# Kernel tuning notes

Hardware: AMD Instinct MI355X
Metric: run time of the kernel (lower is better)

The kernel has to match this reference:

```python
import jax, jax.numpy as jnp
import numpy as np

B, T, N = 4, 6, 1024          # patients, visits, diagnosis codes
CS, GS, H, AT, DA = 48, 32, 270, 32, 64  # code_size, graph_size, hidden, t_attention, dot-attn size
E, L, EV, ED = 32, 32, 20000, 400        # events/visit, event seq len, event vocab, event emb dim
OUT = 4000
INV_SQRT_AT = 1.0 / float(np.sqrt(AT))


def _w(k, shape, s=0.1):
    return jax.random.normal(k, shape, jnp.float32) * s


def setup_inputs():
    key = jax.random.key(0)
    ks = jax.random.split(key, 40)
    cat = jax.random.randint(ks[0], (B, T, N), 0, 4)  # disjoint m1/m2/m3 masks
    return {
        'code_x': jax.random.randint(ks[1], (B, T, N), 0, 2).astype(jnp.int32),
        'divided': jnp.stack([cat == 1, cat == 2, cat == 3], axis=-1).astype(jnp.int32),
        'neighbors': jax.random.randint(ks[2], (B, T, N), 0, 2).astype(jnp.int32),
        'lens': jnp.full((B,), T, dtype=jnp.int32),
        'events': jax.random.randint(ks[3], (B, T, E, L), 0, EV).astype(jnp.int32),
        'c_emb': _w(ks[4], (N, CS)),
        'n_emb': _w(ks[5], (N, CS)),
        'u_emb': _w(ks[6], (N, GS)),
        'adj': (jax.random.uniform(ks[7], (N, N)) < 0.02).astype(jnp.float32),
        'Wg': _w(ks[8], (CS, GS), 0.05), 'bg': jnp.zeros((GS,), jnp.float32),
        'gru_Wih': _w(ks[9], (GS, 3 * H), 0.05),
        'gru_Whh': _w(ks[10], (H, 3 * H), 0.05),
        'gru_bih': jnp.zeros((3 * H,), jnp.float32),
        'gru_bhh': jnp.zeros((3 * H,), jnp.float32),
        'Wq': _w(ks[11], (GS, AT), 0.05), 'bq': jnp.zeros((AT,), jnp.float32),
        'Wk': _w(ks[12], (GS, AT), 0.05), 'bk': jnp.zeros((AT,), jnp.float32),
        'Wv': _w(ks[13], (GS, H), 0.05), 'bv': jnp.zeros((H,), jnp.float32),
        'Wd': _w(ks[14], (H, DA), 0.05), 'bd': jnp.zeros((DA,), jnp.float32),
        'ctx': _w(ks[15], (DA,), 0.1),
        'Eemb': _w(ks[16], (EV, ED), 0.1),
        'lstm_Wih': _w(ks[17], (ED, 4 * H), 0.05),
        'lstm_Whh': _w(ks[18], (H, 4 * H), 0.05),
        'lstm_b': jnp.zeros((4 * H,), jnp.float32),
        'Wc': _w(ks[19], (H, OUT), 0.05),
        'bc': jnp.zeros((OUT,), jnp.float32),
    }


def _forward(code_x, divided, neighbors, events,
             c_emb, n_emb, u_emb, adj, Wg, bg,
             gru_Wih, gru_Whh, gru_bih, gru_bhh,
             Wq, bq, Wk, bk, Wv, bv,
             Wd, bd, ctx,
             Eemb, lstm_Wih, lstm_Whh, lstm_b,
             Wc, bc):
    Bsz, Tn, Nn = code_x.shape
    Hh = gru_Whh.shape[0]
    cx = code_x.astype(jnp.float32)
    nb = neighbors.astype(jnp.float32)
    dv = divided.astype(jnp.float32)

    def gru_cell(x, h):  # torch GRUCell: gates in (r, z, n) order
        gi = x @ gru_Wih + gru_bih
        gh = h @ gru_Whh + gru_bhh
        ir, iz, i_n = jnp.split(gi, 3, axis=-1)
        hr, hz, h_n = jnp.split(gh, 3, axis=-1)
        r = jax.nn.sigmoid(ir + hr)
        z = jax.nn.sigmoid(iz + hz)
        n = jnp.tanh(i_n + r * h_n)
        return (1.0 - z) * n + z * h

    def visit_step(carry, xs):
        h_prev, no_prev = carry
        t, c_t, n_t, d_t = xs  # c_t/n_t: [B,N], d_t: [B,N,3]
        cm = c_t[..., None]
        nm = n_t[..., None]
        # GraphLayer
        ce = cm * c_emb  # [B,N,CS]
        ne = nm * n_emb
        Ace = jnp.einsum('mn,bnc->bmc', adj, ce)
        Ane = jnp.einsum('mn,bnc->bmc', adj, ne)
        co = jax.nn.leaky_relu((ce + cm * Ace + cm * Ane) @ Wg + bg)  # [B,N,GS]
        no = jax.nn.leaky_relu((ne + nm * Ane + nm * Ace) @ Wg + bg)
        m1 = d_t[..., 0] > 0
        m2 = d_t[..., 1] > 0
        m3 = d_t[..., 2] > 0
        # TransitionLayer: persistent codes (m1) -> GRU, masked max-pool
        h_m1 = gru_cell(co, h_prev)  # [B,N,H]
        has1 = jnp.any(m1, axis=1, keepdims=True)
        mx1 = jnp.max(jnp.where(m1[..., None], h_m1, -jnp.inf), axis=1)
        out_m1 = jnp.where(has1, mx1, 0.0)
        # emerging (m2) / unrelated (m3) codes -> single-head attention over the m23 set
        m23 = m2 | m3
        q_in = jnp.where(m3[..., None], u_emb, no_prev)  # [B,N,GS]
        q = q_in @ Wq + bq
        k = co @ Wk + bk
        v = co @ Wv + bv
        g = jnp.einsum('bia,bja->bij', q, k) * INV_SQRT_AT  # [B,N,N]
        has23 = jnp.any(m23, axis=1)  # [B]
        g = jnp.where(m23[:, None, :], g, -jnp.inf)
        g = jnp.where(has23[:, None, None], g, 0.0)  # keep softmax finite when m23 empty
        score = jax.nn.softmax(g, axis=-1)
        h_m23 = jnp.tanh(jnp.einsum('bij,bjh->bih', score, v))  # [B,N,H]
        valid23 = (t > 0) & has23
        mx23 = jnp.max(jnp.where(m23[..., None], h_m23, -jnp.inf), axis=1)
        out_m23 = jnp.where(valid23[:, None], mx23, 0.0)
        h_new = jnp.where(m1[..., None], h_m1, 0.0)
        h_new = jnp.where(((t > 0) & m23)[..., None], h_m23, h_new)
        return (h_new, no), out_m1 + out_m23

    h0 = jnp.zeros((Bsz, Nn, Hh), jnp.float32)
    no0 = jnp.zeros((Bsz, Nn, GS), jnp.float32)
    xs = (jnp.arange(Tn), jnp.swapaxes(cx, 0, 1), jnp.swapaxes(nb, 0, 1), jnp.swapaxes(dv, 0, 1))
    _, outs = jax.lax.scan(visit_step, (h0, no0), xs)
    out_last = outs[-1]  # only the last visit's output survives the original loop

    # SentimentModel: embedding + LSTM over last visit's events (seqs == padded length L)
    x_emb = Eemb[events[:, -1]]  # [B,E,L,ED]

    def lstm_step(carry, x_t):  # torch LSTM gate order (i, f, g, o)
        h, c = carry
        gates = x_t @ lstm_Wih + h @ lstm_Whh + lstm_b
        i, f, gg, o = jnp.split(gates, 4, axis=-1)
        c = jax.nn.sigmoid(f) * c + jax.nn.sigmoid(i) * jnp.tanh(gg)
        h = jax.nn.sigmoid(o) * jnp.tanh(c)
        return (h, c), None

    hc0 = (jnp.zeros((Bsz, E, Hh), jnp.float32), jnp.zeros((Bsz, E, Hh), jnp.float32))
    (h_ev, _), _ = jax.lax.scan(lstm_step, hc0, jnp.moveaxis(x_emb, 2, 0))  # [B,E,H]

    def dp_attention(x):  # x: [B,M,H] -> [B,H]
        vu = (x @ Wd + bd) @ ctx  # [B,M]
        s = jax.nn.softmax(vu, axis=-1)
        return jnp.sum(x * s[..., None], axis=-2)

    stacked = jnp.concatenate([out_last[:, None, :], h_ev], axis=1)  # [B,1+E,H]
    o1 = dp_attention(stacked)
    o2 = dp_attention(o1[:, None, :])  # softmax over a singleton -> identity (as in source)
    return jax.nn.sigmoid(o2 @ Wc + bc)  # [B,OUT]


def reference(code_x, divided, neighbors, lens, events,
              c_emb, n_emb, u_emb, adj, Wg, bg,
              gru_Wih, gru_Whh, gru_bih, gru_bhh,
              Wq, bq, Wk, bk, Wv, bv,
              Wd, bd, ctx,
              Eemb, lstm_Wih, lstm_Whh, lstm_b,
              Wc, bc):
    # lens is all-T (fixed number of visits per patient in this reference)
    return _forward(code_x, divided, neighbors, events,
                    c_emb, n_emb, u_emb, adj, Wg, bg,
                    gru_Wih, gru_Whh, gru_bih, gru_bhh,
                    Wq, bq, Wk, bk, Wv, bv,
                    Wd, bd, ctx,
                    Eemb, lstm_Wih, lstm_Whh, lstm_b,
                    Wc, bc)
```

## Files before the change

kernel.cpp:

```cpp
#include <hip/hip_runtime.h>
#include <hip/hip_bf16.h>
#include <math.h>

#define Bc   4
#define Tc   6
#define Nc   1024
#define CSc  48
#define GSc  32
#define Hc   270
#define ATc  32
#define DAc  64
#define Ec   32
#define Lc   32
#define EDc  400
#define OUTc 4000
#define H3c  810
#define H4c  1080
#define BEc  128
#define KPE  416
#define KPG  64
#define KAB  320
#define NCMB 1382
#define NZCAP 96
#define INV_SQRT_AT_F 0.17677669529663687f

typedef unsigned short ushort_t;
using s8v  = __attribute__((ext_vector_type(8))) short;
using f4v  = __attribute__((ext_vector_type(4))) float;
using u16x8= __attribute__((ext_vector_type(8))) unsigned short;

__device__ __forceinline__ float sigmoid_f(float x){ return 1.0f/(1.0f+expf(-x)); }
__device__ __forceinline__ ushort_t f2bf(float x){
    __hip_bfloat16 b = __float2bfloat16(x);
    return *reinterpret_cast<ushort_t*>(&b);
}
__device__ __forceinline__ float b2f(ushort_t u){
    return __uint_as_float(((unsigned int)u)<<16);
}

template<int EPIL, int SPLITK, int ASEL>
__global__ __launch_bounds__(256)
void mfma_k(const ushort_t* __restrict__ A, const ushort_t* __restrict__ BT,
            const float* __restrict__ bias,
            void* __restrict__ P0, void* __restrict__ P1, void* __restrict__ P2,
            const float* __restrict__ PF, const int* __restrict__ DV,
            const int* __restrict__ DV2,
            int M, int N, int Kp, int lda, int ldb, int ldc,
            long long sA, long long sB, long long sC, int tpar)
{
    __shared__ ushort_t As[128*40];
    __shared__ ushort_t Bs[128*40];
    const int z = blockIdx.z;
    int kbeg = 0, kend = Kp;
    if (SPLITK > 0){
        int ks = Kp / SPLITK;
        kbeg = z*ks; kend = kbeg + ks;
    } else {
        if (ASEL == 0) A += (size_t)z * (size_t)sA;
        BT += (size_t)z * (size_t)sB;
    }
    const int m0 = blockIdx.y*128, n0 = blockIdx.x*128;
    const int tid = threadIdx.x;
    const int w = tid>>6, l = tid&63;
    const int wm = (w>>1)*64, wn = (w&1)*64;
    const int lr = l&15, lk = (l>>4)*8, lq = l>>4;
    const int srow = tid>>2, kseg = tid&3;

    f4v acc[4][4];
    #pragma unroll
    for (int mi=0;mi<4;mi++)
      #pragma unroll
      for (int ni=0;ni<4;ni++)
        acc[mi][ni] = (f4v){0.0f,0.0f,0.0f,0.0f};

    for (int k0=kbeg;k0<kend;k0+=32){
        #pragma unroll
        for (int i=0;i<2;i++){
            int row = srow + i*64;
            int ga = m0+row;
            uint4 va = make_uint4(0u,0u,0u,0u);
            if (ga < M){
                if (ASEL == 2){
                    int isno = ga >> 12;
                    int r = ga & 4095; int b = r >> 10, n = r & 1023;
                    int kk = k0 + kseg*8;
                    if (kk < CSc){
                        const float* emb = isno ? (const float*)P2 : (const float*)A;
                        const int*   msk = isno ? DV2 : DV;
                        float m = (float)msk[((size_t)b*Tc + tpar)*Nc + n];
                        f4v e0 = *(const f4v*)(emb + (size_t)n*CSc + kk);
                        f4v e1 = *(const f4v*)(emb + (size_t)n*CSc + kk + 4);
                        f4v s0 = *(const f4v*)(PF + (size_t)n*(Bc*CSc) + b*CSc + kk);
                        f4v s1 = *(const f4v*)(PF + (size_t)n*(Bc*CSc) + b*CSc + kk + 4);
                        u16x8 tmp;
                        #pragma unroll
                        for (int j=0;j<4;j++) tmp[j]   = f2bf(m*(e0[j]+s0[j]));
                        #pragma unroll
                        for (int j=0;j<4;j++) tmp[4+j] = f2bf(m*(e1[j]+s1[j]));
                        va = *(uint4*)&tmp;
                    }
                } else if (ASEL == 3){
                    int ll = ga >> 7, be = ga & 127; int b = be >> 5, e = be & 31;
                    int kk = k0 + kseg*8;
                    if (kk < EDc){
                        int ev = DV[(((size_t)b*Tc + (Tc-1))*Ec + e)*Lc + ll];
                        const float* src = PF + (size_t)ev*EDc + kk;
                        f4v e0 = *(const f4v*)src;
                        f4v e1 = *(const f4v*)(src + 4);
                        u16x8 tmp;
                        #pragma unroll
                        for (int j=0;j<4;j++) tmp[j]   = f2bf(e0[j]);
                        #pragma unroll
                        for (int j=0;j<4;j++) tmp[4+j] = f2bf(e1[j]);
                        va = *(uint4*)&tmp;
                    }
                } else {
                    va = *(const uint4*)(A + (size_t)ga*lda + k0 + kseg*8);
                }
            }
            *(uint4*)&As[row*40 + kseg*8] = va;
            int gb = n0+row;
            uint4 vb = make_uint4(0u,0u,0u,0u);
            if (gb < N) vb = *(const uint4*)(BT + (size_t)gb*ldb + k0 + kseg*8);
            *(uint4*)&Bs[row*40 + kseg*8] = vb;
        }
        __syncthreads();
        s8v af[4], bfr[4];
        #pragma unroll
        for (int mi=0;mi<4;mi++) af[mi]  = *(const s8v*)&As[(wm+mi*16+lr)*40 + lk];
        #pragma unroll
        for (int ni=0;ni<4;ni++) bfr[ni] = *(const s8v*)&Bs[(wn+ni*16+lr)*40 + lk];
        #pragma unroll
        for (int mi=0;mi<4;mi++)
          #pragma unroll
          for (int ni=0;ni<4;ni++)
            acc[mi][ni] = __builtin_amdgcn_mfma_f32_16x16x32_bf16(af[mi], bfr[ni], acc[mi][ni], 0,0,0);
        __syncthreads();
    }

    #pragma unroll
    for (int mi=0;mi<4;mi++){
      #pragma unroll
      for (int ni=0;ni<4;ni++){
        int col = n0+wn+ni*16+lr;
        if (col >= N) continue;
        float bv_ = bias ? bias[col] : 0.0f;
        #pragma unroll
        for (int r=0;r<4;r++){
          int row = m0+wm+mi*16+lq*4+r;
          if (row >= M) continue;
          float x = acc[mi][ni][r] + bv_;
          if (EPIL == 0){
              float* C = (float*)P0;
              size_t base = (SPLITK>0) ? (size_t)z*(size_t)sC : 0;
              size_t grow = (SPLITK>0) ? (size_t)row : (size_t)z*M + row;
              C[base + grow*ldc + col] = x;
          } else if (EPIL == 1){
              x = (x>0.0f) ? x : 0.01f*x;
              if (row < 4096) ((ushort_t*)P0)[(size_t)row*KAB + col] = f2bf(x);
              else            ((ushort_t*)P1)[(size_t)(row-4096)*32 + col] = f2bf(x);
          } else if (EPIL == 5){
              int b2 = row>>10, rh = row&1023;
              if (col < 32){
                  int kt = rh>>7, nt_=(rh>>4)&7, lrK=rh&15, lqK=col>>3, e=col&7;
                  ((ushort_t*)P0)[((((size_t)b2*8+kt)*8+nt_)*64 + lqK*16+lrK)*8 + e] = f2bf(x);
              } else if (col < 302){
                  int vd = col-32;
                  int c = rh>>5, lqV=(rh>>3)&3, e=rh&7, nt=vd>>4, lrV=vd&15;
                  ((ushort_t*)P1)[((((size_t)b2*32+c)*18+nt)*64 + lqV*16+lrV)*8 + e] = f2bf(x);
              } else {
                  ((float*)P2)[(size_t)row*H4c + (col-302)] = x;
              }
          }
        }
      }
    }
}

__global__ __launch_bounds__(256)
void attn_fused_kernel(const ushort_t* __restrict__ no_prev, const ushort_t* __restrict__ u_embb,
                       const float* __restrict__ Wq, const float* __restrict__ bq,
                       const ushort_t* __restrict__ kSw, const ushort_t* __restrict__ vSw,
                       const int* __restrict__ divided, const float* __restrict__ hm1,
                       ushort_t* __restrict__ Abuf, float* __restrict__ hm23,
                       int t, int wr23)
{
    __shared__ ushort_t Pb[32*16*40];
    __shared__ ushort_t Qs[16*40];
    __shared__ float    mskS[1024];
    __shared__ float    redS[4][16];
    __shared__ float    hasS[4];
    float* qinS = (float*)Pb;
    float* WqS  = (float*)&Pb[1056];

    const int rt = blockIdx.x;
    const int b  = blockIdx.y;
    const int tid = threadIdx.x;
    const int w = tid>>6, l = tid&63, lr = l&15, lq = l>>4;
    const int lk8 = lq*8;
    const int row0 = rt*16;
    const size_t gq = (size_t)b*Nc + row0;

    bool lany = false;
    #pragma unroll
    for (int c4=0;c4<4;c4++){
        int c = tid*4 + c4;
        const int* dv = divided + (((size_t)b*Tc + t)*Nc + c)*3;
        bool m23 = (dv[1]>0)||(dv[2]>0);
        mskS[c] = m23 ? 1.0f : 0.0f;
        lany |= m23;
    }
    bool wany = __any(lany);
    if (l==0) hasS[w] = wany ? 1.0f : 0.0f;

    for (int i=tid;i<16*32;i+=256){
        int r = i>>5, j = i&31;
        int n = row0 + r;
        bool m3 = divided[(((size_t)b*Tc+t)*Nc+n)*3+2] > 0;
        qinS[r*33+j] = m3 ? b2f(u_embb[(size_t)n*GSc+j]) : b2f(no_prev[(gq+r)*GSc+j]);
    }
    for (int i=tid;i<32*32;i+=256){
        int j=i>>5, o=i&31;
        WqS[j*33+o] = Wq[(size_t)j*ATc+o];
    }
    __syncthreads();
    const bool has = (hasS[0]+hasS[1]+hasS[2]+hasS[3]) > 0.5f;

    {
        int r = tid>>4, o2 = (tid&15)*2;
        float a0 = bq[o2], a1 = bq[o2+1];
        for (int j=0;j<32;j++){
            float q = qinS[r*33+j];
            a0 += q*WqS[j*33+o2];
            a1 += q*WqS[j*33+o2+1];
        }
        Qs[r*40+o2]   = f2bf(a0);
        Qs[r*40+o2+1] = f2bf(a1);
    }
    __syncthreads();

    s8v af = *(const s8v*)&Qs[lr*40 + lk8];
    s8v kf[8][2];
    #pragma unroll
    for (int kt=0;kt<8;kt++)
      #pragma unroll
      for (int ni=0;ni<2;ni++)
        kf[kt][ni] = *(const s8v*)(kSw + ((((size_t)b*8+kt)*8 + (w*2+ni))*64 + l)*8);
    f4v qk[8][2];
    #pragma unroll
    for (int kt=0;kt<8;kt++)
      #pragma unroll
      for (int ni=0;ni<2;ni++){
        f4v zz = (f4v){0,0,0,0};
        qk[kt][ni] = __builtin_amdgcn_mfma_f32_16x16x32_bf16(af, kf[kt][ni], zz, 0,0,0);
      }

    float rmax[4] = {-INFINITY,-INFINITY,-INFINITY,-INFINITY};
    #pragma unroll
    for (int kt=0;kt<8;kt++)
      #pragma unroll
      for (int ni=0;ni<2;ni++){
        int colb = kt*128 + (w*2+ni)*16 + lr;
        float mk = mskS[colb];
        #pragma unroll
        for (int r2=0;r2<4;r2++){
            float v = qk[kt][ni][r2]*INV_SQRT_AT_F;
            qk[kt][ni][r2] = v;
            if (mk > 0.5f) rmax[r2] = fmaxf(rmax[r2], v);
        }
      }
    #pragma unroll
    for (int o=1;o<16;o<<=1)
      #pragma unroll
      for (int r2=0;r2<4;r2++) rmax[r2] = fmaxf(rmax[r2], __shfl_xor(rmax[r2], o, 64));
    if (lr==0){
        #pragma unroll
        for (int r2=0;r2<4;r2++) redS[w][lq*4+r2] = rmax[r2];
    }
    __syncthreads();
    float gm[4], inv[4];
    #pragma unroll
    for (int r2=0;r2<4;r2++){
        float m = fmaxf(fmaxf(redS[0][lq*4+r2], redS[1][lq*4+r2]),
                        fmaxf(redS[2][lq*4+r2], redS[3][lq*4+r2]));
        gm[r2] = m;
    }
    float rs[4] = {0,0,0,0};
    #pragma unroll
    for (int kt=0;kt<8;kt++)
      #pragma unroll
      for (int ni=0;ni<2;ni++){
        int colb = kt*128 + (w*2+ni)*16 + lr;
        float mk = mskS[colb];
        #pragma unroll
        for (int r2=0;r2<4;r2++){
            float p = (mk > 0.5f) ? expf(qk[kt][ni][r2] - gm[r2]) : 0.0f;
            qk[kt][ni][r2] = p;
            rs[r2] += p;
        }
      }
    #pragma unroll
    for (int o=1;o<16;o<<=1)
      #pragma unroll
      for (int r2=0;r2<4;r2++) rs[r2] += __shfl_xor(rs[r2], o, 64);
    __syncthreads();
    if (lr==0){
        #pragma unroll
        for (int r2=0;r2<4;r2++) redS[w][lq*4+r2] = rs[r2];
    }
    __syncthreads();
    #pragma unroll
    for (int r2=0;r2<4;r2++){
        float s = redS[0][lq*4+r2] + redS[1][lq*4+r2] + redS[2][lq*4+r2] + redS[3][lq*4+r2];
        inv[r2] = has ? 1.0f/s : 0.0f;
    }

    #pragma unroll
    for (int kt=0;kt<8;kt++)
      #pragma unroll
      for (int ni=0;ni<2;ni++)
        #pragma unroll
        for (int r2=0;r2<4;r2++)
            Pb[(kt*4+w)*640 + (lq*4+r2)*40 + ni*16+lr] = f2bf(qk[kt][ni][r2]*inv[r2]);
    __syncthreads();

    f4v acc[5];
    #pragma unroll
    for (int j5=0;j5<5;j5++) acc[j5] = (f4v){0,0,0,0};
    for (int c=0;c<32;c++){
        s8v pa = *(const s8v*)&Pb[c*640 + lr*40 + lk8];
        #pragma unroll
        for (int j5=0;j5<5;j5++){
            int nt = w + 4*j5;
            if (nt < 18){
                s8v vf = *(const s8v*)(vSw + ((((size_t)b*32+c)*18 + nt)*64 + l)*8);
                acc[j5] = __builtin_amdgcn_mfma_f32_16x16x32_bf16(pa, vf, acc[j5], 0,0,0);
            }
        }
    }

    #pragma unroll
    for (int j5=0;j5<5;j5++){
        int nt = w + 4*j5;
        if (nt >= 18) continue;
        int col = nt*16 + lr;
        if (col >= Hc) continue;
        #pragma unroll
        for (int r2=0;r2<4;r2++){
            int row16 = lq*4 + r2;
            size_t grow = gq + row16;
            int n = row0 + row16;
            const int* dv = divided + (((size_t)b*Tc + t)*Nc + n)*3;
            bool m1  = dv[0]>0;
            bool m23 = (dv[1]>0)||(dv[2]>0);
            float xt = tanhf(acc[j5][r2]);
            float hv = m23 ? xt : (m1 ? hm1[grow*Hc + col] : 0.0f);
            Abuf[grow*KAB + 32 + col] = f2bf(hv);
            if (wr23) hm23[grow*Hc + col] = xt;
        }
    }
}

template<int ACT>
__global__ __launch_bounds__(256)
void gemm_kernel(const float* __restrict__ A, const float* __restrict__ Bm,
                 const float* __restrict__ bias, float* __restrict__ C,
                 int M, int Nn, int K)
{
    constexpr int BM=64, BN=64, BK=16;
    __shared__ float As[BK][BM+4];
    __shared__ float Bs[BK][BN+4];
    const int row0 = blockIdx.y*BM, col0 = blockIdx.x*BN;
    const int tid = threadIdx.x;
    const int tr = (tid>>4)<<2;
    const int tc = (tid&15)<<2;
    const int ar = tid>>2;
    const int ac = (tid&3)<<2;
    const int br = tid>>4;
    const int bc = (tid&15)<<2;
    float acc[4][4] = {};
    for (int k0=0;k0<K;k0+=BK){
        #pragma unroll
        for (int i=0;i<4;i++){
            int gr=row0+ar, gc=k0+ac+i;
            As[ac+i][ar] = (gr<M && gc<K) ? A[(size_t)gr*K+gc] : 0.0f;
        }
        #pragma unroll
        for (int i=0;i<4;i++){
            int gr=k0+br, gc=col0+bc+i;
            Bs[br][bc+i] = (gr<K && gc<Nn) ? Bm[(size_t)gr*Nn+gc] : 0.0f;
        }
        __syncthreads();
        #pragma unroll
        for (int kk=0;kk<BK;kk++){
            float a0=As[kk][tr+0], a1=As[kk][tr+1], a2=As[kk][tr+2], a3=As[kk][tr+3];
            float b0=Bs[kk][tc+0], b1=Bs[kk][tc+1], b2=Bs[kk][tc+2], b3=Bs[kk][tc+3];
            acc[0][0]+=a0*b0; acc[0][1]+=a0*b1; acc[0][2]+=a0*b2; acc[0][3]+=a0*b3;
            acc[1][0]+=a1*b0; acc[1][1]+=a1*b1; acc[1][2]+=a1*b2; acc[1][3]+=a1*b3;
            acc[2][0]+=a2*b0; acc[2][1]+=a2*b1; acc[2][2]+=a2*b2; acc[2][3]+=a2*b3;
            acc[3][0]+=a3*b0; acc[3][1]+=a3*b1; acc[3][2]+=a3*b2; acc[3][3]+=a3*b3;
        }
        __syncthreads();
    }
    #pragma unroll
    for (int i=0;i<4;i++){
        int r=row0+tr+i; if (r>=M) continue;
        #pragma unroll
        for (int j=0;j<4;j++){
            int c=col0+tc+j; if (c>=Nn) continue;
            float x = acc[i][j];
            if (bias) x += bias[c];
            if (ACT==3) x = 1.0f/(1.0f+expf(-x));
            C[(size_t)r*Nn+c] = x;
        }
    }
}

#define PR0 32768LL
#define PR1 2048LL
#define PR3 442240LL
#define PR4 1382LL
#define PR5 449280LL
#define PR6 313344LL
#define PR7 73728LL
#define PR8 36864LL
#define PR9 1310720LL
#define PR10 1179648LL
#define PRTOT (PR0+PR1+PR3+PR4+PR5+PR6+PR7+PR8+PR9+PR10)

__global__ void prep_kernel(const float* __restrict__ u_emb,
                            const float* __restrict__ Wg,
                            const float* __restrict__ Wk, const float* __restrict__ Wv,
                            const float* __restrict__ gru_Wih, const float* __restrict__ gru_Whh,
                            const float* __restrict__ bk, const float* __restrict__ bv,
                            const float* __restrict__ gru_bih, const float* __restrict__ gru_bhh,
                            const float* __restrict__ lstm_Wih, const float* __restrict__ lstm_Whh,
                            ushort_t* u_embb, ushort_t* WgT,
                            ushort_t* WB, float* biasB, ushort_t* WTl, ushort_t* WhhRT,
                            ushort_t* hbLA, ushort_t* hbLB, float* cst, ushort_t* Abuf,
                            ushort_t* vSw)
{
    long long idx = (long long)blockIdx.x*256 + threadIdx.x;
    if (idx < PR0){ u_embb[idx] = f2bf(u_emb[idx]); return; } idx -= PR0;
    if (idx < PR1){ int n=(int)(idx>>6), k=(int)(idx&63);
        WgT[idx] = (k<CSc) ? f2bf(Wg[(size_t)k*GSc+n]) : (ushort_t)0; return; } idx -= PR1;
    if (idx < PR3){
        int n=(int)(idx/KAB), k=(int)(idx%KAB);
        float v = 0.0f;
        if (n < 32){            if (k<32) v = Wk[(size_t)k*ATc + n]; }
        else if (n < 302){      if (k<32) v = Wv[(size_t)k*Hc + (n-32)]; }
        else if (n < 572){ int j=n-302;
            if (k<32) v = gru_Wih[(size_t)k*H3c + j];
            else if (k<302) v = gru_Whh[(size_t)(k-32)*H3c + j]; }
        else if (n < 842){ int j=(n-572)+270;
            if (k<32) v = gru_Wih[(size_t)k*H3c + j];
            else if (k<302) v = gru_Whh[(size_t)(k-32)*H3c + j]; }
        else if (n < 1112){ int j=(n-842)+540;
            if (k<32) v = gru_Wih[(size_t)k*H3c + j]; }
        else { int j=(n-1112)+540;
            if (k>=32 && k<302) v = gru_Whh[(size_t)(k-32)*H3c + j]; }
        WB[idx] = f2bf(v); return; } idx -= PR3;
    if (idx < PR4){
        int n = (int)idx; float v;
        if (n < 32)        v = bk[n];
        else if (n < 302)  v = bv[n-32];
        else if (n < 572)  v = gru_bih[n-302] + gru_bhh[n-302];
        else if (n < 842)  v = gru_bih[(n-572)+270] + gru_bhh[(n-572)+270];
        else if (n < 1112) v = gru_bih[(n-842)+540];
        else               v = gru_bhh[(n-1112)+540];
        biasB[n] = v; return; } idx -= PR4;
    if (idx < PR5){ int n=(int)(idx/KPE), k=(int)(idx%KPE);
        WTl[idx] = (k<EDc) ? f2bf(lstm_Wih[(size_t)k*H4c+n]) : (ushort_t)0; return; } idx -= PR5;
    if (idx < PR6){
        int jg=(int)(idx/(64*288)); int r2=(int)(idx%(64*288));
        int n=r2/288, k=r2%288;
        int gate=n>>4, jj=n&15, j=jg*16+jj;
        WhhRT[idx] = (k<Hc && j<Hc) ? f2bf(lstm_Whh[(size_t)k*H4c + gate*Hc + j]) : (ushort_t)0;
        return; } idx -= PR6;
    if (idx < PR7){ if (idx < 36864) hbLA[idx] = 0; else hbLB[idx-36864] = 0; return; } idx -= PR7;
    if (idx < PR8){ cst[idx] = 0.0f; return; } idx -= PR8;
    if (idx < PR9){ Abuf[idx] = 0; return; } idx -= PR9;
    if (idx < PR10){ vSw[idx] = 0; }
}

__global__ void nz_build_kernel(const float* __restrict__ adj, int* __restrict__ nzc,
                                int* __restrict__ nzidx)
{
    int n = blockIdx.x;
    __shared__ int cnt;
    if (threadIdx.x == 0) cnt = 0;
    __syncthreads();
    for (int k = threadIdx.x; k < Nc; k += 256){
        if (adj[(size_t)n*Nc + k] != 0.0f){
            int pos = atomicAdd(&cnt, 1);
            if (pos < NZCAP) nzidx[(size_t)n*NZCAP + pos] = k;
        }
    }
    __syncthreads();
    if (threadIdx.x == 0) nzc[n] = (cnt < NZCAP) ? cnt : NZCAP;
}

__global__ __launch_bounds__(192)
void s_sparse_kernel(const int* __restrict__ code_x, const int* __restrict__ neighbors,
                     const float* __restrict__ c_emb, const float* __restrict__ n_emb,
                     const int* __restrict__ nzc, const int* __restrict__ nzidx,
                     int t, float* __restrict__ S)
{
    int n = blockIdx.x;
    int tid = threadIdx.x;
    int b = tid / CSc, c = tid % CSc;
    int cnt = nzc[n];
    float s = 0.0f;
    for (int i=0; i<cnt; i++){
        int k = nzidx[(size_t)n*NZCAP + i];
        int cm = code_x  [((size_t)b*Tc+t)*Nc + k];
        int nm = neighbors[((size_t)b*Tc+t)*Nc + k];
        float e = 0.0f;
        if (cm) e += c_emb[(size_t)k*CSc + c];
        if (nm) e += n_emb[(size_t)k*CSc + c];
        s += e;
    }
    S[(size_t)n*(Bc*CSc) + tid] = s;
}

__global__ void gru_combine_kernel(const float* __restrict__ gsum, const ushort_t* __restrict__ Abuf,
                                   float* __restrict__ hm1)
{
    int r = blockIdx.x;
    const float* G = gsum + (size_t)r*H4c;
    for (int j = threadIdx.x; j < Hc; j += blockDim.x){
        float rg = sigmoid_f(G[j]);
        float zg = sigmoid_f(G[270+j]);
        float ng = tanhf(G[540+j] + rg*G[810+j]);
        float h  = b2f(Abuf[(size_t)r*KAB + 32 + j]);
        hm1[(size_t)r*Hc + j] = (1.0f-zg)*ng + zg*h;
    }
}

__global__ void gru_combine_t0_kernel(const float* __restrict__ gsum, const int* __restrict__ divided,
                                      ushort_t* __restrict__ Abuf)
{
    int r = blockIdx.x;
    int b = r >> 10, n = r & 1023;
    bool m1 = divided[(((size_t)b*Tc+0)*Nc+n)*3 + 0] > 0;
    const float* G = gsum + (size_t)r*H4c;
    for (int j = threadIdx.x; j < Hc; j += blockDim.x){
        float rg = sigmoid_f(G[j]);
        float zg = sigmoid_f(G[270+j]);
        float ng = tanhf(G[540+j] + rg*G[810+j]);
        float hv = (1.0f-zg)*ng;
        Abuf[(size_t)r*KAB + 32 + j] = m1 ? f2bf(hv) : (ushort_t)0;
    }
}

__global__ __launch_bounds__(320)
void outlast_partial_kernel(const int* __restrict__ divided,
                            const float* __restrict__ hm1, const float* __restrict__ hm23,
                            float* __restrict__ part1, float* __restrict__ part23)
{
    int nc = blockIdx.x, b = blockIdx.y;
    int j = threadIdx.x;
    if (j >= Hc) return;
    float m1v = -INFINITY, m23v = -INFINITY;
    #pragma unroll 4
    for (int n = nc*32; n < nc*32+32; n++){
        const int* dv = divided + (((size_t)b*Tc + (Tc-1))*Nc + n)*3;
        bool m1  = dv[0] > 0;
        bool m23 = (dv[1] > 0) || (dv[2] > 0);
        size_t o = ((size_t)b*Nc+n)*Hc + j;
        if (m1)  m1v  = fmaxf(m1v,  hm1[o]);
        if (m23) m23v = fmaxf(m23v, hm23[o]);
    }
    part1 [((size_t)b*32+nc)*320 + j] = m1v;
    part23[((size_t)b*32+nc)*320 + j] = m23v;
}

__global__ __launch_bounds__(320)
void outlast_combine_kernel(const float* __restrict__ part1, const float* __restrict__ part23,
                            float* __restrict__ outlast)
{
    int b = blockIdx.x; int j = threadIdx.x;
    if (j >= Hc) return;
    float a = -INFINITY, c = -INFINITY;
    for (int nc=0;nc<32;nc++){
        a = fmaxf(a, part1 [((size_t)b*32+nc)*320 + j]);
        c = fmaxf(c, part23[((size_t)b*32+nc)*320 + j]);
    }
    outlast[(size_t)b*Hc + j] = (a==-INFINITY ? 0.0f : a) + (c==-INFINITY ? 0.0f : c);
}

__global__ __launch_bounds__(256)
void lstm_step_mfma(const float* __restrict__ gx,
                    const ushort_t* __restrict__ WhhRT,
                    const ushort_t* __restrict__ hb_in,
                    ushort_t* __restrict__ hb_out,
                    float* __restrict__ cst,
                    float* __restrict__ hev_out)
{
    int cg = blockIdx.x & 3, jg = blockIdx.x >> 2;
    int tid = threadIdx.x;
    int w = tid>>6, l = tid&63;
    int mi = w>>1, ni0 = (w&1)*2;
    int arow = cg*32 + mi*16 + (l&15);
    int koff = (l>>4)*8;
    const ushort_t* Wb = WhhRT + (size_t)jg*64*288;

    f4v acc0 = (f4v){0,0,0,0}, acc1 = (f4v){0,0,0,0};
    #pragma unroll
    for (int k0=0;k0<288;k0+=32){
        s8v a  = *(const s8v*)(hb_in + (size_t)arow*288 + k0 + koff);
        s8v b0 = *(const s8v*)(Wb + (size_t)(ni0*16 + (l&15))*288 + k0 + koff);
        s8v b1 = *(const s8v*)(Wb + (size_t)((ni0+1)*16 + (l&15))*288 + k0 + koff);
        acc0 = __builtin_amdgcn_mfma_f32_16x16x32_bf16(a, b0, acc0, 0,0,0);
        acc1 = __builtin_amdgcn_mfma_f32_16x16x32_bf16(a, b1, acc1, 0,0,0);
    }
    __shared__ float gs[32][64];
    int crow = mi*16 + (l>>4)*4;
    int ccol = l&15;
    #pragma unroll
    for (int r=0;r<4;r++){
        gs[crow+r][ni0*16 + ccol]     = acc0[r];
        gs[crow+r][(ni0+1)*16 + ccol] = acc1[r];
    }
    __syncthreads();
    #pragma unroll
    for (int p=0;p<2;p++){
        int idx = tid + p*256;
        int cl = idx>>4, jj = idx&15;
        int j = jg*16 + jj;
        if (j < Hc){
            int cell = cg*32 + cl;
            const float* g = gx + (size_t)cell*H4c;
            float ig = sigmoid_f(gs[cl][jj]      + g[j]);
            float fg = sigmoid_f(gs[cl][16+jj]   + g[Hc+j]);
            float gg = tanhf    (gs[cl][32+jj]   + g[2*Hc+j]);
            float og = sigmoid_f(gs[cl][48+jj]   + g[3*Hc+j]);
            size_t co = (size_t)cell*288 + j;
            float cn = fg*cst[co] + ig*gg;
            cst[co] = cn;
            float hn = og*tanhf(cn);
            hb_out[co] = f2bf(hn);
            if (hev_out) hev_out[(size_t)cell*Hc + j] = hn;
        }
    }
}

__global__ __launch_bounds__(256)
void heads_kernel(const float* __restrict__ outlast, const float* __restrict__ hev,
                  const float* __restrict__ Wd, const float* __restrict__ bd,
                  const float* __restrict__ ctx, float* __restrict__ o1)
{
    int b = blockIdx.x, tid = threadIdx.x;
    __shared__ float wdc[Hc+1];
    __shared__ float sc[Ec+1];
    for (int j=tid;j<Hc;j+=256){
        float s = 0.0f;
        for (int d=0;d<DAc;d++) s += Wd[(size_t)j*DAc+d]*ctx[d];
        wdc[j] = s;
    }
    if (tid == 255){
        float s = 0.0f;
        for (int d=0;d<DAc;d++) s += bd[d]*ctx[d];
        wdc[Hc] = s;
    }
    __syncthreads();
    if (tid < Ec+1){
        const float* x = (tid==0) ? (outlast + (size_t)b*Hc)
                                  : (hev + ((size_t)b*Ec + tid-1)*Hc);
        float s = wdc[Hc];
        for (int j=0;j<Hc;j++) s += x[j]*wdc[j];
        sc[tid] = s;
    }
    __syncthreads();
    if (tid == 0){
        float m = -INFINITY;
        for (int s=0;s<Ec+1;s++) m = fmaxf(m, sc[s]);
        float sum = 0.0f;
        for (int s=0;s<Ec+1;s++){ sc[s] = expf(sc[s]-m); sum += sc[s]; }
        float inv = 1.0f/sum;
        for (int s=0;s<Ec+1;s++) sc[s] *= inv;
    }
    __syncthreads();
    for (int j=tid;j<Hc;j+=256){
        float acc = sc[0]*outlast[(size_t)b*Hc + j];
        for (int e=0;e<Ec;e++) acc += sc[1+e]*hev[((size_t)b*Ec+e)*Hc + j];
        o1[(size_t)b*Hc + j] = acc;
    }
}

extern "C" void kernel_launch(void* const* d_in, const int* in_sizes, int n_in,
                              void* d_out, int out_size, void* d_ws, size_t ws_size,
                              hipStream_t stream)
{
    const int*   code_x    = (const int*)d_in[0];
    const int*   divided   = (const int*)d_in[1];
    const int*   neighbors = (const int*)d_in[2];
    const int*   events    = (const int*)d_in[4];
    const float* c_emb     = (const float*)d_in[5];
    const float* n_emb     = (const float*)d_in[6];
    const float* u_emb     = (const float*)d_in[7];
    const float* adj       = (const float*)d_in[8];
    const float* Wg        = (const float*)d_in[9];
    const float* bg        = (const float*)d_in[10];
    const float* gru_Wih   = (const float*)d_in[11];
    const float* gru_Whh   = (const float*)d_in[12];
    const float* gru_bih   = (const float*)d_in[13];
    const float* gru_bhh   = (const float*)d_in[14];
    const float* Wq        = (const float*)d_in[15];
    const float* bq        = (const float*)d_in[16];
    const float* Wk        = (const float*)d_in[17];
    const float* bk        = (const float*)d_in[18];
    const float* Wv        = (const float*)d_in[19];
    const float* bv        = (const float*)d_in[20];
    const float* Wd        = (const float*)d_in[21];
    const float* bd        = (const float*)d_in[22];
    const float* ctx       = (const float*)d_in[23];
    const float* Eemb      = (const float*)d_in[24];
    const float* lstm_Wih  = (const float*)d_in[25];
    const float* lstm_Whh  = (const float*)d_in[26];
    const float* lstm_b    = (const float*)d_in[27];
    const float* Wc        = (const float*)d_in[28];
    const float* bc        = (const float*)d_in[29];
    float* out = (float*)d_out;

    float* ws = (float*)d_ws;
    size_t off = 0;
    auto alloc = [&](size_t n){ n = (n+7)&~(size_t)7; float* p = ws + off; off += n; return p; };
    auto allocU = [&](size_t n){ return (ushort_t*)alloc((n+1)/2); };

    float* hm1     = alloc((size_t)Bc*Nc*Hc);
    float* hm23    = alloc((size_t)Bc*Nc*Hc);
    float* S       = alloc((size_t)Nc*Bc*CSc);
    float* gsum    = alloc((size_t)Bc*Nc*H4c);
    ushort_t* Abuf  = allocU((size_t)Bc*Nc*KAB);
    ushort_t* noA   = allocU((size_t)Bc*Nc*GSc);
    ushort_t* noB   = allocU((size_t)Bc*Nc*GSc);
    ushort_t* kSw   = allocU((size_t)Bc*Nc*ATc);
    ushort_t* vSw   = allocU((size_t)Bc*32*18*64*8);
    ushort_t* u_embb= allocU((size_t)Nc*GSc);
    ushort_t* WgT   = allocU((size_t)GSc*KPG);
    ushort_t* WB    = allocU((size_t)NCMB*KAB);
    ushort_t* WTl   = allocU((size_t)H4c*KPE);
    ushort_t* WhhRT = allocU((size_t)17*64*288);
    ushort_t* hbLA  = allocU((size_t)BEc*288);
    ushort_t* hbLB  = allocU((size_t)BEc*288);
    float* cst     = alloc((size_t)BEc*288);
    float* biasB   = alloc((size_t)NCMB);
    int*   nzc     = (int*)alloc((size_t)Nc);
    int*   nzidx   = (int*)alloc((size_t)Nc*NZCAP);
    float* outlast = alloc((size_t)Bc*Hc);
    float* o1      = alloc((size_t)Bc*Hc);
    float* hev     = alloc((size_t)BEc*Hc);
    float* part1   = alloc((size_t)Bc*32*320);
    float* part23  = alloc((size_t)Bc*32*320);

    float* gatesx  = gsum;
    (void)ws_size; (void)in_sizes; (void)n_in; (void)out_size;

    {
        long long nb = (PRTOT + 255) / 256;
        prep_kernel<<<dim3((unsigned)nb), dim3(256), 0, stream>>>(
            u_emb, Wg, Wk, Wv, gru_Wih, gru_Whh, bk, bv, gru_bih, gru_bhh,
            lstm_Wih, lstm_Whh,
            u_embb, WgT, WB, biasB, WTl, WhhRT, hbLA, hbLB, cst, Abuf, vSw);
        nz_build_kernel<<<dim3(Nc), dim3(256), 0, stream>>>(adj, nzc, nzidx);
    }

    ushort_t* no_prev = noB;
    ushort_t* no_cur  = noA;
    for (int t=0; t<Tc; t++){
        s_sparse_kernel<<<dim3(Nc), dim3(192), 0, stream>>>(code_x, neighbors, c_emb, n_emb,
                                                            nzc, nzidx, t, S);
        mfma_k<1,0,2><<<dim3(1,64,1),256,0,stream>>>(
            (const ushort_t*)c_emb, WgT, bg,
            Abuf, no_cur, (void*)n_emb, S, code_x, neighbors,
            2*Bc*Nc, GSc, KPG, 0, KPG, 0, 0,0,0, t);
        mfma_k<5,0,0><<<dim3(11,32,1),256,0,stream>>>(
            Abuf, WB, biasB,
            kSw, vSw, gsum, nullptr, nullptr, nullptr,
            Bc*Nc, NCMB, KAB, KAB, KAB, 0, 0,0,0, 0);
        if (t == 0){
            gru_combine_t0_kernel<<<dim3(Bc*Nc), dim3(256), 0, stream>>>(gsum, divided, Abuf);
        } else {
            gru_combine_kernel<<<dim3(Bc*Nc), dim3(256), 0, stream>>>(gsum, Abuf, hm1);
            attn_fused_kernel<<<dim3(64, Bc), dim3(256), 0, stream>>>(
                no_prev, u_embb, Wq, bq, kSw, vSw, divided, hm1,
                Abuf, hm23, t, (t == Tc-1) ? 1 : 0);
            if (t == Tc-1){
                outlast_partial_kernel<<<dim3(32, Bc), dim3(320), 0, stream>>>(divided, hm1, hm23, part1, part23);
                outlast_combine_kernel<<<dim3(Bc), dim3(320), 0, stream>>>(part1, part23, outlast);
            }
        }
        ushort_t* tmp = no_prev; no_prev = no_cur; no_cur = tmp;
    }

    mfma_k<0,0,3><<<dim3(9,32,1),256,0,stream>>>(
        nullptr, WTl, lstm_b,
        gatesx, nullptr, nullptr, Eemb, events, nullptr,
        BEc*Lc, H4c, KPE, 0, KPE, H4c, 0,0,0, 0);
    {
        ushort_t* hin = hbLA; ushort_t* hout = hbLB;
        for (int l=0; l<Lc; l++){
            lstm_step_mfma<<<dim3(68), dim3(256), 0, stream>>>(
                gatesx + (size_t)l*BEc*H4c, WhhRT, hin, hout, cst,
                (l == Lc-1) ? hev : nullptr);
            ushort_t* tmp = hin; hin = hout; hout = tmp;
        }
    }

    heads_kernel<<<dim3(Bc), dim3(256), 0, stream>>>(outlast, hev, Wd, bd, ctx, o1);
    {
        dim3 grid((OUTc+63)/64, 1, 1);
        gemm_kernel<3><<<grid,dim3(256),0,stream>>>(o1, Wc, bc, out, Bc, OUTc, Hc);
    }
}
```

Measured before the change: 1.055 ms.

## Replace small MFMA GEMM with scalar kernel; halve attention rows per block

Replaces the tiny code/neighbor embedding GEMM (8192x32, K=48) with a dedicated scalar kernel that stages Wg in shared memory and applies leaky ReLU inline. The GRU combine now writes the m1/zero hidden state into Abuf directly and only stores hm1 on the last step. The attention kernel then writes only m23 rows and no longer reads hm1. The attention kernel processes 8 rows per block instead of 16, doubling the grid for more parallelism but wasting half the MFMA tile rows.

```diff
diff --git a/kernel.cpp b/kernel.cpp
--- a/kernel.cpp
+++ b/kernel.cpp
@@ -80,26 +80,7 @@
             int ga = m0+row;
             uint4 va = make_uint4(0u,0u,0u,0u);
             if (ga < M){
-                if (ASEL == 2){
-                    int isno = ga >> 12;
-                    int r = ga & 4095; int b = r >> 10, n = r & 1023;
-                    int kk = k0 + kseg*8;
-                    if (kk < CSc){
-                        const float* emb = isno ? (const float*)P2 : (const float*)A;
-                        const int*   msk = isno ? DV2 : DV;
-                        float m = (float)msk[((size_t)b*Tc + tpar)*Nc + n];
-                        f4v e0 = *(const f4v*)(emb + (size_t)n*CSc + kk);
-                        f4v e1 = *(const f4v*)(emb + (size_t)n*CSc + kk + 4);
-                        f4v s0 = *(const f4v*)(PF + (size_t)n*(Bc*CSc) + b*CSc + kk);
-                        f4v s1 = *(const f4v*)(PF + (size_t)n*(Bc*CSc) + b*CSc + kk + 4);
-                        u16x8 tmp;
-                        #pragma unroll
-                        for (int j=0;j<4;j++) tmp[j]   = f2bf(m*(e0[j]+s0[j]));
-                        #pragma unroll
-                        for (int j=0;j<4;j++) tmp[4+j] = f2bf(m*(e1[j]+s1[j]));
-                        va = *(uint4*)&tmp;
-                    }
-                } else if (ASEL == 3){
+                if (ASEL == 3){
                     int ll = ga >> 7, be = ga & 127; int b = be >> 5, e = be & 31;
                     int kk = k0 + kseg*8;
                     if (kk < EDc){
@@ -155,10 +136,6 @@
               size_t base = (SPLITK>0) ? (size_t)z*(size_t)sC : 0;
               size_t grow = (SPLITK>0) ? (size_t)row : (size_t)z*M + row;
               C[base + grow*ldc + col] = x;
-          } else if (EPIL == 1){
-              x = (x>0.0f) ? x : 0.01f*x;
-              if (row < 4096) ((ushort_t*)P0)[(size_t)row*KAB + col] = f2bf(x);
-              else            ((ushort_t*)P1)[(size_t)(row-4096)*32 + col] = f2bf(x);
           } else if (EPIL == 5){
               int b2 = row>>10, rh = row&1023;
               if (col < 32){
@@ -178,10 +155,43 @@
 }
 
 __global__ __launch_bounds__(256)
+void cono_kernel(const int* __restrict__ code_x, const int* __restrict__ neighbors,
+                 const float* __restrict__ c_emb, const float* __restrict__ n_emb,
+                 const float* __restrict__ S, const float* __restrict__ Wg,
+                 const float* __restrict__ bg, int t,
+                 ushort_t* __restrict__ Abuf, ushort_t* __restrict__ no_cur)
+{
+    __shared__ float X[8][48];
+    __shared__ float Wgs[48][32];
+    __shared__ float bgs[32];
+    int bk = blockIdx.x, tid = threadIdx.x;
+    for (int i=tid;i<48*32;i+=256) Wgs[i>>5][i&31] = Wg[i];
+    if (tid < 32) bgs[tid] = bg[tid];
+    if (tid < 192){
+        int q = tid/48, k = tid%48;
+        int r = bk*4+q; int b = r>>10, n = r&1023;
+        float cm = (float)code_x  [((size_t)b*Tc+t)*Nc + n];
+        float nm = (float)neighbors[((size_t)b*Tc+t)*Nc + n];
+        float s  = S[(size_t)n*(Bc*CSc) + b*CSc + k];
+        X[q][k]   = cm*(c_emb[(size_t)n*CSc+k] + s);
+        X[4+q][k] = nm*(n_emb[(size_t)n*CSc+k] + s);
+    }
+    __syncthreads();
+    int slot = tid>>5, c = tid&31;
+    float a = bgs[c];
+    #pragma unroll
+    for (int k=0;k<48;k++) a += X[slot][k]*Wgs[k][c];
+    a = (a>0.0f) ? a : 0.01f*a;
+    int r = bk*4 + (slot&3);
+    if (slot < 4) Abuf[(size_t)r*KAB + c] = f2bf(a);
+    else          no_cur[(size_t)r*GSc + c] = f2bf(a);
+}
+
+__global__ __launch_bounds__(256)
 void attn_fused_kernel(const ushort_t* __restrict__ no_prev, const ushort_t* __restrict__ u_embb,
                        const float* __restrict__ Wq, const float* __restrict__ bq,
                        const ushort_t* __restrict__ kSw, const ushort_t* __restrict__ vSw,
-                       const int* __restrict__ divided, const float* __restrict__ hm1,
+                       const int* __restrict__ divided,
                        ushort_t* __restrict__ Abuf, float* __restrict__ hm23,
                        int t, int wr23)
 {
@@ -198,7 +208,7 @@
     const int tid = threadIdx.x;
     const int w = tid>>6, l = tid&63, lr = l&15, lq = l>>4;
     const int lk8 = lq*8;
-    const int row0 = rt*16;
+    const int row0 = rt*8;
     const size_t gq = (size_t)b*Nc + row0;
 
     bool lany = false;
@@ -213,8 +223,8 @@
     bool wany = __any(lany);
     if (l==0) hasS[w] = wany ? 1.0f : 0.0f;
 
-    for (int i=tid;i<16*32;i+=256){
-        int r = i>>5, j = i&31;
+    if (tid < 8*32){
+        int r = tid>>5, j = tid&31;
         int n = row0 + r;
         bool m3 = divided[(((size_t)b*Tc+t)*Nc+n)*3+2] > 0;
         qinS[r*33+j] = m3 ? b2f(u_embb[(size_t)n*GSc+j]) : b2f(no_prev[(gq+r)*GSc+j]);
@@ -228,11 +238,14 @@
 
     {
         int r = tid>>4, o2 = (tid&15)*2;
-        float a0 = bq[o2], a1 = bq[o2+1];
-        for (int j=0;j<32;j++){
-            float q = qinS[r*33+j];
-            a0 += q*WqS[j*33+o2];
-            a1 += q*WqS[j*33+o2+1];
+        float a0 = 0.0f, a1 = 0.0f;
+        if (r < 8){
+            a0 = bq[o2]; a1 = bq[o2+1];
+            for (int j=0;j<32;j++){
+                float q = qinS[r*33+j];
+                a0 += q*WqS[j*33+o2];
+                a1 += q*WqS[j*33+o2+1];
+            }
         }
         Qs[r*40+o2]   = f2bf(a0);
         Qs[r*40+o2+1] = f2bf(a1);
@@ -327,6 +340,7 @@
     f4v acc[5];
     #pragma unroll
     for (int j5=0;j5<5;j5++) acc[j5] = (f4v){0,0,0,0};
+    #pragma unroll 4
     for (int c=0;c<32;c++){
         s8v pa = *(const s8v*)&Pb[c*640 + lr*40 + lk8];
         #pragma unroll
@@ -348,14 +362,13 @@
         #pragma unroll
         for (int r2=0;r2<4;r2++){
             int row16 = lq*4 + r2;
+            if (row16 >= 8) continue;
             size_t grow = gq + row16;
             int n = row0 + row16;
             const int* dv = divided + (((size_t)b*Tc + t)*Nc + n)*3;
-            bool m1  = dv[0]>0;
             bool m23 = (dv[1]>0)||(dv[2]>0);
             float xt = tanhf(acc[j5][r2]);
-            float hv = m23 ? xt : (m1 ? hm1[grow*Hc + col] : 0.0f);
-            Abuf[grow*KAB + 32 + col] = f2bf(hv);
+            if (m23) Abuf[grow*KAB + 32 + col] = f2bf(xt);
             if (wr23) hm23[grow*Hc + col] = xt;
         }
     }
@@ -523,17 +536,25 @@
     S[(size_t)n*(Bc*CSc) + tid] = s;
 }
 
-__global__ void gru_combine_kernel(const float* __restrict__ gsum, const ushort_t* __restrict__ Abuf,
-                                   float* __restrict__ hm1)
+__global__ void gru_combine_kernel(const float* __restrict__ gsum, ushort_t* __restrict__ Abuf,
+                                   const int* __restrict__ divided, float* __restrict__ hm1,
+                                   int t)
 {
     int r = blockIdx.x;
+    int b = r >> 10, n = r & 1023;
+    const int* dv = divided + (((size_t)b*Tc+t)*Nc+n)*3;
+    bool m1  = dv[0] > 0;
+    bool m23 = (dv[1] > 0) || (dv[2] > 0);
+    bool last = (t == Tc-1);
     const float* G = gsum + (size_t)r*H4c;
     for (int j = threadIdx.x; j < Hc; j += blockDim.x){
         float rg = sigmoid_f(G[j]);
         float zg = sigmoid_f(G[270+j]);
         float ng = tanhf(G[540+j] + rg*G[810+j]);
         float h  = b2f(Abuf[(size_t)r*KAB + 32 + j]);
-        hm1[(size_t)r*Hc + j] = (1.0f-zg)*ng + zg*h;
+        float hv = (1.0f-zg)*ng + zg*h;
+        if (!m23) Abuf[(size_t)r*KAB + 32 + j] = m1 ? f2bf(hv) : (ushort_t)0;
+        if (last) hm1[(size_t)r*Hc + j] = hv;
     }
 }
 
@@ -771,10 +792,8 @@
     for (int t=0; t<Tc; t++){
         s_sparse_kernel<<<dim3(Nc), dim3(192), 0, stream>>>(code_x, neighbors, c_emb, n_emb,
                                                             nzc, nzidx, t, S);
-        mfma_k<1,0,2><<<dim3(1,64,1),256,0,stream>>>(
-            (const ushort_t*)c_emb, WgT, bg,
-            Abuf, no_cur, (void*)n_emb, S, code_x, neighbors,
-            2*Bc*Nc, GSc, KPG, 0, KPG, 0, 0,0,0, t);
+        cono_kernel<<<dim3(1024), dim3(256), 0, stream>>>(
+            code_x, neighbors, c_emb, n_emb, S, Wg, bg, t, Abuf, no_cur);
         mfma_k<5,0,0><<<dim3(11,32,1),256,0,stream>>>(
             Abuf, WB, biasB,
             kSw, vSw, gsum, nullptr, nullptr, nullptr,
@@ -782,9 +801,9 @@
         if (t == 0){
             gru_combine_t0_kernel<<<dim3(Bc*Nc), dim3(256), 0, stream>>>(gsum, divided, Abuf);
         } else {
-            gru_combine_kernel<<<dim3(Bc*Nc), dim3(256), 0, stream>>>(gsum, Abuf, hm1);
-            attn_fused_kernel<<<dim3(64, Bc), dim3(256), 0, stream>>>(
-                no_prev, u_embb, Wq, bq, kSw, vSw, divided, hm1,
+            gru_combine_kernel<<<dim3(Bc*Nc), dim3(256), 0, stream>>>(gsum, Abuf, divided, hm1, t);
+            attn_fused_kernel<<<dim3(128, Bc), dim3(256), 0, stream>>>(
+                no_prev, u_embb, Wq, bq, kSw, vSw, divided,
                 Abuf, hm23, t, (t == Tc-1) ? 1 : 0);
             if (t == Tc-1){
                 outlast_partial_kernel<<<dim3(32, Bc), dim3(320), 0, stream>>>(divided, hm1, hm23, part1, part23);
```

Measured after the change: 1.045 ms. No clear change (-0.9%).
